# Optimization experiments

Measured on AMD Instinct MI355X. Metric: run time of the kernel, lower is better.

The kernel has to match this reference:

```python
import jax, jax.numpy as jnp
import numpy as np

N_NODES = 50000
N_EDGES = 800000
IN_FEATS = 64
K = 4
OUT_FEATS = 256


def setup_inputs() -> dict:
    key = jax.random.key(0)
    k1, k2, k3, k4, k5 = jax.random.split(key, 5)
    signal = jax.random.normal(k1, (N_NODES, IN_FEATS), dtype=jnp.float32)
    src = jax.random.randint(k2, (N_EDGES,), 0, N_NODES, dtype=jnp.int32)
    dst = jax.random.randint(k3, (N_EDGES,), 0, N_NODES, dtype=jnp.int32)
    lambda_max = jnp.array([2.0], dtype=jnp.float32)  # normalized Laplacian bound
    W = jax.random.normal(k4, (IN_FEATS * K, OUT_FEATS), dtype=jnp.float32) * (1.0 / np.sqrt(IN_FEATS * K))
    b = jax.random.normal(k5, (OUT_FEATS,), dtype=jnp.float32) * 0.01
    return {"signal": signal, "src": src, "dst": dst, "lambda_max": lambda_max, "W": W, "b": b}


def reference(signal, src, dst, lambda_max, W, b):
    n = signal.shape[0]
    # in-degrees, clamped to >= 1, then D^{-1/2}
    deg = jax.ops.segment_sum(jnp.ones_like(dst, dtype=signal.dtype), dst, num_segments=n)
    d_sqrt = jnp.power(jnp.clip(deg, 1.0), -0.5)[:, None]  # [N,1]

    def unn_laplacian(x):
        # D^{-1/2} A D^{-1/2} x via gather-from-src, scatter-sum-to-dst
        h = (x * d_sqrt)[src]                                   # [E,f]
        agg = jax.ops.segment_sum(h, dst, num_segments=n)       # [N,f]
        return agg * d_sqrt

    X0 = signal
    Xs = [X0]
    if K > 1:
        re_norm = 2.0 / lambda_max  # broadcasts over nodes ([1] -> [N,f])
        X1 = -re_norm * unn_laplacian(X0) + X0 * (re_norm - 1.0)
        Xs.append(X1)
        for _ in range(2, K):
            Xi = -2.0 * re_norm * unn_laplacian(X1) + X1 * 2.0 * (re_norm - 1.0) - X0
            Xs.append(Xi)
            X1, X0 = Xi, X1
    Xt = jnp.concatenate(Xs, axis=1)  # [N, f*K]
    return jax.nn.relu(Xt @ W + b)
```

## Files before the change

kernel.cpp:

```cpp
#include <hip/hip_runtime.h>

#define NN 50000
#define NE 800000
#define F  64
#define FK 256
#define OUTF 256
#define CAP 48
#define NT 3128
#define NBKT 196
#define NBLK 196
#define EB 4096

typedef __attribute__((ext_vector_type(8))) short s16x8;
typedef __attribute__((ext_vector_type(4))) float f32x4;

static __device__ __forceinline__ unsigned short f2bf(float f) {
    unsigned u = __float_as_uint(f);
    u += 0x7fffu + ((u >> 16) & 1u);
    return (unsigned short)(u >> 16);
}
static __device__ __forceinline__ float bf2f(int h) {
    return __uint_as_float(((unsigned)(h & 0xffff)) << 16);
}


__global__ __launch_bounds__(1024) void histk(const int* __restrict__ dst,
                                              int* __restrict__ blockhist) {
    __shared__ int h[NBKT];
    int t = threadIdx.x, blk = blockIdx.x;
    if (t < NBKT) h[t] = 0;
    __syncthreads();
    int e0 = blk * EB;
    for (int i = t; i < EB; i += 1024) {
        int e = e0 + i;
        if (e < NE) atomicAdd(&h[dst[e] >> 8], 1);
    }
    __syncthreads();
    if (t < NBKT) blockhist[t * NBLK + blk] = h[t];
}

__global__ __launch_bounds__(256) void scank(const int* __restrict__ blockhist,
                                             int* __restrict__ blockpre,
                                             int* __restrict__ colsum) {
    __shared__ int v[256];
    int t = threadIdx.x, b = blockIdx.x;
    int x = (t < NBLK) ? blockhist[b * NBLK + t] : 0;
    v[t] = x;
    __syncthreads();
    for (int off = 1; off < 256; off <<= 1) {
        int y = (t >= off) ? v[t - off] : 0;
        __syncthreads();
        v[t] += y;
        __syncthreads();
    }
    if (t < NBLK) blockpre[b * NBLK + t] = v[t] - x;
    if (t == 255) colsum[b] = v[255];
}

__global__ __launch_bounds__(256) void bbasek(const int* __restrict__ colsum,
                                              int* __restrict__ bucketbase) {
    __shared__ int v[256];
    int t = threadIdx.x;
    int x = (t < NBKT) ? colsum[t] : 0;
    v[t] = x;
    __syncthreads();
    for (int off = 1; off < 256; off <<= 1) {
        int y = (t >= off) ? v[t - off] : 0;
        __syncthreads();
        v[t] += y;
        __syncthreads();
    }
    if (t < NBKT) bucketbase[t] = v[t] - x;
}

__global__ __launch_bounds__(1024) void scatk(const int* __restrict__ src,
                                              const int* __restrict__ dst,
                                              const int* __restrict__ blockpre,
                                              const int* __restrict__ bucketbase,
                                              unsigned* __restrict__ ebuf) {
    __shared__ int h[NBKT];
    __shared__ int rk[NBKT];
    __shared__ int gb[NBKT];
    __shared__ int s[256];
    __shared__ unsigned sv[EB];
    __shared__ int sg[EB];
    int t = threadIdx.x, blk = blockIdx.x;
    int e0 = blk * EB;
    if (t < NBKT) h[t] = 0;
    __syncthreads();
    for (int i = t; i < EB; i += 1024) {
        int e = e0 + i;
        if (e < NE) atomicAdd(&h[dst[e] >> 8], 1);
    }
    __syncthreads();
    if (t < 256) s[t] = (t < NBKT) ? h[t] : 0;
    __syncthreads();
    for (int off = 1; off < 256; off <<= 1) {
        int y = (t < 256 && t >= off) ? s[t - off] : 0;
        __syncthreads();
        if (t < 256) s[t] += y;
        __syncthreads();
    }
    if (t < NBKT) {
        int ex = s[t] - h[t];
        rk[t] = ex;
        gb[t] = bucketbase[t] + blockpre[t * NBLK + blk] - ex;
    }
    __syncthreads();
    for (int i = t; i < EB; i += 1024) {
        int e = e0 + i;
        if (e < NE) {
            int d = dst[e];
            int bkt = d >> 8;
            int pos = atomicAdd(&rk[bkt], 1);
            sv[pos] = (unsigned)src[e] | ((unsigned)(d & 255) << 16);
            sg[pos] = gb[bkt] + pos;
        }
    }
    __syncthreads();
    int nloc = min(EB, NE - e0);
    for (int i = t; i < nloc; i += 1024)
        ebuf[sg[i]] = sv[i];
}

__global__ __launch_bounds__(256) void buildk(const unsigned* __restrict__ ebuf,
                                              const int* __restrict__ bucketbase,
                                              const int* __restrict__ colsum,
                                              int* __restrict__ cnt,
                                              float* __restrict__ dsq,
                                              int* __restrict__ csr) {
    __shared__ int lcnt[256];
    __shared__ int lcsr[256 * CAP];
    int b = blockIdx.x, t = threadIdx.x;
    lcnt[t] = 0;
    __syncthreads();
    int base = bucketbase[b];
    int m = colsum[b];
    for (int i = t; i < m; i += 256) {
        unsigned v = ebuf[base + i];
        int dl = (int)((v >> 16) & 255u);
        int k = atomicAdd(&lcnt[dl], 1);
        if (k < CAP) lcsr[dl * CAP + k] = (int)(v & 0xFFFFu);
    }
    __syncthreads();
    int n0 = b * 256;
    if (n0 + t < NN) {
        int c = lcnt[t];
        cnt[n0 + t] = c;
        dsq[n0 + t] = rsqrtf(fmaxf((float)c, 1.0f));
    }
    for (int i = t; i < 256 * CAP; i += 256) {
        int node = n0 + i / CAP;
        if (node < NN) csr[(size_t)n0 * CAP + i] = lcsr[i];
    }
}


__global__ void copy0_kernel(const float* __restrict__ sig,
                             unsigned short* __restrict__ XrowH,
                             unsigned short* __restrict__ XrowL,
                             unsigned short* __restrict__ XfH) {
    int i = blockIdx.x * blockDim.x + threadIdx.x;
    if (i >= NN * 16) return;
    int n = i >> 4, fq = i & 15;
    float4 v = *(const float4*)&sig[n * F + fq * 4];
    unsigned short h0 = f2bf(v.x), h1 = f2bf(v.y), h2 = f2bf(v.z), h3 = f2bf(v.w);
    unsigned short l0 = f2bf(v.x - bf2f(h0)), l1 = f2bf(v.y - bf2f(h1));
    unsigned short l2 = f2bf(v.z - bf2f(h2)), l3 = f2bf(v.w - bf2f(h3));
    *(ushort4*)&XrowH[(size_t)n * 192 + fq * 4] = make_ushort4(h0, h1, h2, h3);
    *(ushort4*)&XrowL[(size_t)n * 192 + fq * 4] = make_ushort4(l0, l1, l2, l3);
    int t = n >> 4, m = n & 15;
    int k0 = fq >> 3, qq = (fq >> 1) & 3, half = fq & 1;
    size_t base = ((size_t)((t * 8 + k0) * 64 + qq * 16 + m)) * 8 + half * 4;
    *(ushort4*)&XfH[base] = make_ushort4(h0, h1, h2, h3);
}

__global__ void convw_kernel(const float* __restrict__ W,
                             unsigned short* __restrict__ WfH,
                             unsigned short* __restrict__ WfL) {
    int id = blockIdx.x * blockDim.x + threadIdx.x;
    if (id >= 8192) return;
    int lane = id & 63, k0 = (id >> 6) & 7, ct = id >> 9;
    int n = lane & 15, q = lane >> 4;
    s16x8 h, l;
    #pragma unroll
    for (int j = 0; j < 8; ++j) {
        float x = W[(k0 * 32 + q * 8 + j) * OUTF + ct * 16 + n];
        unsigned short hh = f2bf(x);
        h[j] = (short)hh;
        l[j] = (short)f2bf(x - bf2f(hh));
    }
    ((s16x8*)WfH)[id] = h;
    ((s16x8*)WfL)[id] = l;
}

__global__ __launch_bounds__(256) void lap_kernel(const int* __restrict__ cnt,
                                                  const int* __restrict__ csr,
                                                  const float* __restrict__ dsq,
                                                  const float* __restrict__ lm,
                                                  unsigned short* __restrict__ XrowH,
                                                  unsigned short* __restrict__ XrowL,
                                                  unsigned short* __restrict__ XfH, int p) {
    int wid  = (blockIdx.x * blockDim.x + threadIdx.x) >> 6;
    int lane = threadIdx.x & 63;
    int s = lane >> 3;
    int o = lane & 7;
    if (wid >= NN) return;
    int n  = wid;
    int dg = min(cnt[n], CAP);
    int cin = p - 1;

    float acc[8];
    #pragma unroll
    for (int j = 0; j < 8; ++j) acc[j] = 0.f;

    for (int k = s; k < dg; k += 16) {
        int e0 = csr[n * CAP + k];
        bool pr = (k + 8) < dg;
        int e1 = pr ? csr[n * CAP + k + 8] : e0;
        float d0 = dsq[e0];
        float d1 = pr ? dsq[e1] : 0.f;
        s16x8 x0 = *(const s16x8*)&XrowH[((size_t)e0 * 3 + cin) * 64 + o * 8];
        s16x8 x1 = *(const s16x8*)&XrowH[((size_t)e1 * 3 + cin) * 64 + o * 8];
        #pragma unroll
        for (int j = 0; j < 8; ++j)
            acc[j] += bf2f(x0[j]) * d0 + bf2f(x1[j]) * d1;
    }
    #pragma unroll
    for (int j = 0; j < 8; ++j) {
        acc[j] += __shfl_xor(acc[j], 8);
        acc[j] += __shfl_xor(acc[j], 16);
        acc[j] += __shfl_xor(acc[j], 32);
    }

    float rn = 2.0f / lm[0];
    float dn = dsq[n];
    s16x8 xh = *(const s16x8*)&XrowH[((size_t)n * 3 + cin) * 64 + o * 8];
    s16x8 xl = *(const s16x8*)&XrowL[((size_t)n * 3 + cin) * 64 + o * 8];
    float r[8];
    if (p == 1) {
        float c1 = rn - 1.0f;
        #pragma unroll
        for (int j = 0; j < 8; ++j)
            r[j] = -rn * dn * acc[j] + (bf2f(xh[j]) + bf2f(xl[j])) * c1;
    } else {
        s16x8 zh = *(const s16x8*)&XrowH[((size_t)n * 3 + (p - 2)) * 64 + o * 8];
        s16x8 zl = *(const s16x8*)&XrowL[((size_t)n * 3 + (p - 2)) * 64 + o * 8];
        float c1 = 2.0f * (rn - 1.0f);
        #pragma unroll
        for (int j = 0; j < 8; ++j)
            r[j] = -2.0f * rn * dn * acc[j] + (bf2f(xh[j]) + bf2f(xl[j])) * c1
                 - (bf2f(zh[j]) + bf2f(zl[j]));
    }
    s16x8 h;
    #pragma unroll
    for (int j = 0; j < 8; ++j) h[j] = (short)f2bf(r[j]);

    if (s == 0 && p < 3) {
        *(s16x8*)&XrowH[((size_t)n * 3 + p) * 64 + o * 8] = h;
    } else if (s == 1 && p < 3) {
        s16x8 l;
        #pragma unroll
        for (int j = 0; j < 8; ++j) l[j] = (short)f2bf(r[j] - bf2f(h[j]));
        *(s16x8*)&XrowL[((size_t)n * 3 + p) * 64 + o * 8] = l;
    } else if (s == 2) {
        int t = n >> 4, m = n & 15;
        int k0 = p * 2 + (o >> 2), qq = o & 3;
        size_t chunk = (size_t)((t * 8 + k0) * 64 + qq * 16 + m);
        *(s16x8*)&XfH[chunk * 8] = h;
    }
}

__global__ __launch_bounds__(256, 2) void gemm_kernel(const unsigned short* __restrict__ XfH,
                                                      const unsigned short* __restrict__ WfH,
                                                      const unsigned short* __restrict__ WfL,
                                                      const float* __restrict__ b,
                                                      float* __restrict__ out) {
    int lane = threadIdx.x & 63;
    int w    = threadIdx.x >> 6;
    int rh = w & 1, cg = w >> 1;
    int m = lane & 15, q = lane >> 4;
    int rowblk = blockIdx.x >> 1;
    int ch = blockIdx.x & 1;
    int bt0 = rowblk * 8 + rh * 4;
    const s16x8* AH = (const s16x8*)XfH;
    const s16x8* BH = (const s16x8*)WfH;
    const s16x8* BL = (const s16x8*)WfL;

    f32x4 acc[4][4];
    #pragma unroll
    for (int rt = 0; rt < 4; ++rt)
        #pragma unroll
        for (int c = 0; c < 4; ++c) acc[rt][c] = (f32x4){0.f, 0.f, 0.f, 0.f};

    s16x8 a[2][4], bh[2][4], bl[2][4];
    #pragma unroll
    for (int rt = 0; rt < 4; ++rt) a[0][rt] = AH[((bt0 + rt) * 8 + 0) * 64 + lane];
    #pragma unroll
    for (int c = 0; c < 4; ++c) {
        int ct = ch * 8 + cg * 4 + c;
        bh[0][c] = BH[(ct * 8 + 0) * 64 + lane];
        bl[0][c] = BL[(ct * 8 + 0) * 64 + lane];
    }

    #pragma unroll
    for (int k0 = 0; k0 < 8; ++k0) {
        int cur = k0 & 1, nxt = cur ^ 1;
        if (k0 < 7) {
            #pragma unroll
            for (int rt = 0; rt < 4; ++rt)
                a[nxt][rt] = AH[((bt0 + rt) * 8 + k0 + 1) * 64 + lane];
            #pragma unroll
            for (int c = 0; c < 4; ++c) {
                int ct = ch * 8 + cg * 4 + c;
                bh[nxt][c] = BH[(ct * 8 + k0 + 1) * 64 + lane];
                bl[nxt][c] = BL[(ct * 8 + k0 + 1) * 64 + lane];
            }
        }
        #pragma unroll
        for (int c = 0; c < 4; ++c)
            #pragma unroll
            for (int rt = 0; rt < 4; ++rt) {
                acc[rt][c] = __builtin_amdgcn_mfma_f32_16x16x32_bf16(a[cur][rt], bh[cur][c], acc[rt][c], 0, 0, 0);
                acc[rt][c] = __builtin_amdgcn_mfma_f32_16x16x32_bf16(a[cur][rt], bl[cur][c], acc[rt][c], 0, 0, 0);
            }
    }

    #pragma unroll
    for (int rt = 0; rt < 4; ++rt) {
        int rbase = (bt0 + rt) * 16 + q * 4;
        #pragma unroll
        for (int c = 0; c < 4; ++c) {
            int col = (ch * 8 + cg * 4 + c) * 16 + m;
            float bv = b[col];
            #pragma unroll
            for (int i = 0; i < 4; ++i) {
                int r = rbase + i;
                if (r < NN) out[r * OUTF + col] = fmaxf(acc[rt][c][i] + bv, 0.0f);
            }
        }
    }
}

extern "C" void kernel_launch(void* const* d_in, const int* in_sizes, int n_in,
                              void* d_out, int out_size, void* d_ws, size_t ws_size,
                              hipStream_t stream) {
    const float* signal     = (const float*)d_in[0];
    const int*   src        = (const int*)  d_in[1];
    const int*   dst        = (const int*)  d_in[2];
    const float* lambda_max = (const float*)d_in[3];
    const float* W          = (const float*)d_in[4];
    const float* b          = (const float*)d_in[5];
    float* out = (float*)d_out;

    int*      blockhist  = (int*)d_ws;
    int*      blockpre   = blockhist + NBKT * NBLK;
    int*      colsum     = blockpre + NBKT * NBLK;
    int*      bucketbase = colsum + NBKT;
    int*      cnt        = bucketbase + NBKT + 104;
    float*    dsq        = (float*)(cnt + NN);
    int*      csr        = (int*)(dsq + NN);
    unsigned* ebuf       = (unsigned*)(csr + (size_t)NN * CAP);
    unsigned short* XrowH = (unsigned short*)(ebuf + NE);
    unsigned short* XrowL = XrowH + (size_t)NN * 192;
    unsigned short* XfH   = XrowL + (size_t)NN * 192;
    unsigned short* WfH   = XfH + (size_t)NT * 4096;
    unsigned short* WfL   = WfH + 65536;

    histk<<<NBLK, 1024, 0, stream>>>(dst, blockhist);
    scank<<<NBKT, 256, 0, stream>>>(blockhist, blockpre, colsum);
    bbasek<<<1, 256, 0, stream>>>(colsum, bucketbase);
    scatk<<<NBLK, 1024, 0, stream>>>(src, dst, blockpre, bucketbase, ebuf);
    buildk<<<NBKT, 256, 0, stream>>>(ebuf, bucketbase, colsum, cnt, dsq, csr);

    copy0_kernel<<<(NN * 16 + 255) / 256, 256, 0, stream>>>(signal, XrowH, XrowL, XfH);
    convw_kernel<<<32, 256, 0, stream>>>(W, WfH, WfL);

    for (int p = 1; p <= 3; ++p)
        lap_kernel<<<NN / 4, 256, 0, stream>>>(cnt, csr, dsq, lambda_max, XrowH, XrowL, XfH, p);

    gemm_kernel<<<391 * 2, 256, 0, stream>>>(XfH, WfH, WfL, b, out);
}
```

Measured before the change: 263.0 us.

## Drop low-bf16 W split in GEMM and retile to 32x64 row tiles per block

Removes the bf16 high/low split of W, so the GEMM issues one MFMA per tile instead of two and the WfL buffer and its conversion are gone. The GEMM is also retiled: each block now covers 32 row tiles by 4 column tiles, with every wave holding 8 row tiles of accumulators. A loads are no longer double-buffered, and NT is padded to 3136 so the last block's reads stay in bounds. Halving the MFMA work lowers precision, since W keeps only bf16 mantissa bits, which risks larger error against the fp32 reference. The larger accumulator array also raises register pressure.

```diff
diff --git a/kernel.cpp b/kernel.cpp
--- a/kernel.cpp
+++ b/kernel.cpp
@@ -6,7 +6,7 @@
 #define FK 256
 #define OUTF 256
 #define CAP 48
-#define NT 3128
+#define NT 3136
 #define NBKT 196
 #define NBLK 196
 #define EB 4096
@@ -176,22 +176,16 @@
 }
 
 __global__ void convw_kernel(const float* __restrict__ W,
-                             unsigned short* __restrict__ WfH,
-                             unsigned short* __restrict__ WfL) {
+                             unsigned short* __restrict__ WfH) {
     int id = blockIdx.x * blockDim.x + threadIdx.x;
     if (id >= 8192) return;
     int lane = id & 63, k0 = (id >> 6) & 7, ct = id >> 9;
     int n = lane & 15, q = lane >> 4;
-    s16x8 h, l;
-    #pragma unroll
-    for (int j = 0; j < 8; ++j) {
-        float x = W[(k0 * 32 + q * 8 + j) * OUTF + ct * 16 + n];
-        unsigned short hh = f2bf(x);
-        h[j] = (short)hh;
-        l[j] = (short)f2bf(x - bf2f(hh));
-    }
+    s16x8 h;
+    #pragma unroll
+    for (int j = 0; j < 8; ++j)
+        h[j] = (short)f2bf(W[(k0 * 32 + q * 8 + j) * OUTF + ct * 16 + n]);
     ((s16x8*)WfH)[id] = h;
-    ((s16x8*)WfL)[id] = l;
 }
 
 __global__ __launch_bounds__(256) void lap_kernel(const int* __restrict__ cnt,
@@ -271,67 +265,52 @@
     }
 }
 
-__global__ __launch_bounds__(256, 2) void gemm_kernel(const unsigned short* __restrict__ XfH,
-                                                      const unsigned short* __restrict__ WfH,
-                                                      const unsigned short* __restrict__ WfL,
-                                                      const float* __restrict__ b,
-                                                      float* __restrict__ out) {
+__global__ __launch_bounds__(256) void gemm_kernel(const unsigned short* __restrict__ XfH,
+                                                   const unsigned short* __restrict__ WfH,
+                                                   const float* __restrict__ b,
+                                                   float* __restrict__ out) {
     int lane = threadIdx.x & 63;
     int w    = threadIdx.x >> 6;
-    int rh = w & 1, cg = w >> 1;
     int m = lane & 15, q = lane >> 4;
-    int rowblk = blockIdx.x >> 1;
-    int ch = blockIdx.x & 1;
-    int bt0 = rowblk * 8 + rh * 4;
+    int rb = blockIdx.x >> 2;
+    int cg = blockIdx.x & 3;
+    int t0 = rb * 32 + w * 8;
     const s16x8* AH = (const s16x8*)XfH;
     const s16x8* BH = (const s16x8*)WfH;
-    const s16x8* BL = (const s16x8*)WfL;
-
-    f32x4 acc[4][4];
-    #pragma unroll
-    for (int rt = 0; rt < 4; ++rt)
+
+    f32x4 acc[8][4];
+    #pragma unroll
+    for (int rt = 0; rt < 8; ++rt)
         #pragma unroll
         for (int c = 0; c < 4; ++c) acc[rt][c] = (f32x4){0.f, 0.f, 0.f, 0.f};
 
-    s16x8 a[2][4], bh[2][4], bl[2][4];
-    #pragma unroll
-    for (int rt = 0; rt < 4; ++rt) a[0][rt] = AH[((bt0 + rt) * 8 + 0) * 64 + lane];
-    #pragma unroll
-    for (int c = 0; c < 4; ++c) {
-        int ct = ch * 8 + cg * 4 + c;
-        bh[0][c] = BH[(ct * 8 + 0) * 64 + lane];
-        bl[0][c] = BL[(ct * 8 + 0) * 64 + lane];
-    }
+    s16x8 bh[2][4];
+    #pragma unroll
+    for (int c = 0; c < 4; ++c) bh[0][c] = BH[((cg * 4 + c) * 8 + 0) * 64 + lane];
 
     #pragma unroll
     for (int k0 = 0; k0 < 8; ++k0) {
-        int cur = k0 & 1, nxt = cur ^ 1;
+        int cur = k0 & 1;
         if (k0 < 7) {
             #pragma unroll
-            for (int rt = 0; rt < 4; ++rt)
-                a[nxt][rt] = AH[((bt0 + rt) * 8 + k0 + 1) * 64 + lane];
+            for (int c = 0; c < 4; ++c)
+                bh[cur ^ 1][c] = BH[((cg * 4 + c) * 8 + k0 + 1) * 64 + lane];
+        }
+        #pragma unroll
+        for (int rt = 0; rt < 8; ++rt) {
+            s16x8 a = AH[((t0 + rt) * 8 + k0) * 64 + lane];
             #pragma unroll
-            for (int c = 0; c < 4; ++c) {
-                int ct = ch * 8 + cg * 4 + c;
-                bh[nxt][c] = BH[(ct * 8 + k0 + 1) * 64 + lane];
-                bl[nxt][c] = BL[(ct * 8 + k0 + 1) * 64 + lane];
-            }
+            for (int c = 0; c < 4; ++c)
+                acc[rt][c] = __builtin_amdgcn_mfma_f32_16x16x32_bf16(a, bh[cur][c], acc[rt][c], 0, 0, 0);
         }
-        #pragma unroll
-        for (int c = 0; c < 4; ++c)
-            #pragma unroll
-            for (int rt = 0; rt < 4; ++rt) {
-                acc[rt][c] = __builtin_amdgcn_mfma_f32_16x16x32_bf16(a[cur][rt], bh[cur][c], acc[rt][c], 0, 0, 0);
-                acc[rt][c] = __builtin_amdgcn_mfma_f32_16x16x32_bf16(a[cur][rt], bl[cur][c], acc[rt][c], 0, 0, 0);
-            }
-    }
-
-    #pragma unroll
-    for (int rt = 0; rt < 4; ++rt) {
-        int rbase = (bt0 + rt) * 16 + q * 4;
+    }
+
+    #pragma unroll
+    for (int rt = 0; rt < 8; ++rt) {
+        int rbase = (t0 + rt) * 16 + q * 4;
         #pragma unroll
         for (int c = 0; c < 4; ++c) {
-            int col = (ch * 8 + cg * 4 + c) * 16 + m;
+            int col = (cg * 4 + c) * 16 + m;
             float bv = b[col];
             #pragma unroll
             for (int i = 0; i < 4; ++i) {
@@ -365,7 +344,6 @@
     unsigned short* XrowL = XrowH + (size_t)NN * 192;
     unsigned short* XfH   = XrowL + (size_t)NN * 192;
     unsigned short* WfH   = XfH + (size_t)NT * 4096;
-    unsigned short* WfL   = WfH + 65536;
 
     histk<<<NBLK, 1024, 0, stream>>>(dst, blockhist);
     scank<<<NBKT, 256, 0, stream>>>(blockhist, blockpre, colsum);
@@ -374,10 +352,10 @@
     buildk<<<NBKT, 256, 0, stream>>>(ebuf, bucketbase, colsum, cnt, dsq, csr);
 
     copy0_kernel<<<(NN * 16 + 255) / 256, 256, 0, stream>>>(signal, XrowH, XrowL, XfH);
-    convw_kernel<<<32, 256, 0, stream>>>(W, WfH, WfL);
+    convw_kernel<<<32, 256, 0, stream>>>(W, WfH);
 
     for (int p = 1; p <= 3; ++p)
         lap_kernel<<<NN / 4, 256, 0, stream>>>(cnt, csr, dsq, lambda_max, XrowH, XrowL, XfH, p);
 
-    gemm_kernel<<<391 * 2, 256, 0, stream>>>(XfH, WfH, WfL, b, out);
-}
+    gemm_kernel<<<98 * 4, 256, 0, stream>>>(XfH, WfH, b, out);
+}
```

Measured after the change: 270.1 us. +2.7%, slower.
